# Kernel optimization log

Measured on AMD Instinct MI355X. Metric: run time of the kernel, lower is better.

The kernel has to match this reference:

```python
import jax, jax.numpy as jnp
import numpy as np

CARD = [3049, 10, 7, 3]
EMB = 16
HID = 64
COV = 10
B = 4096
S = 512
IN_DIM = 1 + COV + len(CARD) * EMB + 1  # 76


def setup_inputs() -> dict:
    key = jax.random.key(0)
    ks = jax.random.split(key, 12)
    target = jax.random.uniform(ks[0], (B, S), dtype=jnp.float32) * 100.0
    covariates = jax.random.normal(ks[1], (B, S, COV), dtype=jnp.float32)
    static_cats = jax.random.randint(ks[2], (B, len(CARD)), 0, 3)
    scale = jax.random.uniform(ks[3], (B, 1), dtype=jnp.float32) * 10.0 + 0.1
    emb0 = jax.random.normal(ks[4], (CARD[0], EMB), dtype=jnp.float32) * 0.1
    emb1 = jax.random.normal(ks[5], (CARD[1], EMB), dtype=jnp.float32) * 0.1
    emb2 = jax.random.normal(ks[6], (CARD[2], EMB), dtype=jnp.float32) * 0.1
    emb3 = jax.random.normal(ks[7], (CARD[3], EMB), dtype=jnp.float32) * 0.1
    w_ih = jax.random.normal(ks[8], (IN_DIM, 4 * HID), dtype=jnp.float32) / np.sqrt(IN_DIM)
    w_hh = jax.random.normal(ks[9], (HID, 4 * HID), dtype=jnp.float32) / np.sqrt(HID)
    bias = jnp.zeros((4 * HID,), dtype=jnp.float32)
    w_out = jax.random.normal(ks[10], (HID, 2), dtype=jnp.float32) / np.sqrt(HID)
    b_out = jnp.zeros((2,), dtype=jnp.float32)
    return dict(target=target, covariates=covariates, static_cats=static_cats,
                scale=scale, emb0=emb0, emb1=emb1, emb2=emb2, emb3=emb3,
                w_ih=w_ih, w_hh=w_hh, bias=bias, w_out=w_out, b_out=b_out)


def reference(target, covariates, static_cats, scale,
              emb0, emb1, emb2, emb3, w_ih, w_hh, bias, w_out, b_out):
    # static embedding concat: [B, 4*EMB]
    static_emb = jnp.concatenate([emb0[static_cats[:, 0]], emb1[static_cats[:, 1]],
                                  emb2[static_cats[:, 2]], emb3[static_cats[:, 3]]], axis=-1)
    log_scale = jnp.log1p(scale)                              # [B, 1]
    static_x = jnp.concatenate([static_emb, log_scale], -1)  # [B, 4*EMB+1]
    # teacher-forced previous scaled target: shifted target/scale, zero at t=0
    ps = target / jnp.maximum(scale, 1e-4)                    # [B, S]
    prev = jnp.concatenate([jnp.zeros_like(ps[:, :1]), ps[:, :-1]], axis=1)

    h0 = jnp.zeros((target.shape[0], w_hh.shape[0]), dtype=target.dtype)

    def step(carry, xs):
        h, c = carry
        p_t, cov_t = xs  # [B], [B, COV]
        x = jnp.concatenate([p_t[:, None], cov_t, static_x], axis=-1)  # [B, IN_DIM]
        gates = x @ w_ih + h @ w_hh + bias
        i, f, g, o = jnp.split(gates, 4, axis=-1)
        i = jax.nn.sigmoid(i)
        f = jax.nn.sigmoid(f)
        g = jnp.tanh(g)
        o = jax.nn.sigmoid(o)
        c = f * c + i * g
        h = o * jnp.tanh(c)
        raw = h @ w_out + b_out                    # [B, 2]
        mu_s = jax.nn.softplus(raw[:, 0]) + 1e-4   # [B]
        al = jax.nn.softplus(raw[:, 1]) + 1e-4     # [B]
        return (h, c), (mu_s, al)

    xs = (prev.T, jnp.swapaxes(covariates, 0, 1))  # time-major
    _, (mu_s, al) = jax.lax.scan(step, (h0, h0), xs)
    mus = mu_s.T * scale   # [B, S]
    alphas = al.T          # [B, S]
    return mus, alphas
```

## Files before the change

### kernel.cpp

```cpp
#include <hip/hip_runtime.h>

#define BB 4096
#define SS 512
#define NG 256
#define BT 16
#define NT 512
#define CH 32
#define HSTR 68
#define PSTR 16
#define SBSTR 264
#define OSTR 33

typedef __bf16 bf16_t;
typedef bf16_t bf16x8 __attribute__((ext_vector_type(8)));
typedef float  f32x4  __attribute__((ext_vector_type(4)));

__device__ __forceinline__ unsigned short f2bf(float x) {
    union { float f; unsigned u; } q{x};
    unsigned r = (q.u + 0x7fffu + ((q.u >> 16) & 1u)) >> 16;
    return (unsigned short)r;
}
__device__ __forceinline__ float bf2f(unsigned short s) {
    union { unsigned u; float f; } q{((unsigned)s) << 16};
    return q.f;
}
#define LOG2E 1.4426950408889634f
__device__ __forceinline__ float frcp_(float x)  { return __builtin_amdgcn_rcpf(x); }
__device__ __forceinline__ float fexp2_(float x) { return __builtin_amdgcn_exp2f(x); }
__device__ __forceinline__ float flog2_(float x) { return __builtin_amdgcn_logf(x); }
__device__ __forceinline__ float softplus_(float x){ return x > 20.0f ? x : 0.6931471805599453f * flog2_(1.0f + fexp2_(LOG2E * x)); }

__global__ __launch_bounds__(NT)
void deepar_kernel(const float* __restrict__ target, const float* __restrict__ cov,
                   const int* __restrict__ cats, const float* __restrict__ scale,
                   const float* __restrict__ emb0, const float* __restrict__ emb1,
                   const float* __restrict__ emb2, const float* __restrict__ emb3,
                   const float* __restrict__ w_ih, const float* __restrict__ w_hh,
                   const float* __restrict__ bias, const float* __restrict__ w_out,
                   const float* __restrict__ b_out, float* __restrict__ out)
{
    __shared__ __attribute__((aligned(16))) unsigned char smemA[2 * CH * BT * PSTR * 2];
    __shared__ __attribute__((aligned(16))) unsigned short hbuf[2][BT][HSTR];
    __shared__ float obuf[2][CH][OSTR];
    __shared__ float inv_s[BT], scl_s[BT];

    unsigned short* pcx   = (unsigned short*)smemA;
    float*          sbias = (float*)smemA;
    float*          sx    = (float*)(smemA + BT * SBSTR * 4);

    const int tid  = threadIdx.x;
    const int b0   = blockIdx.x * BT;
    const int lane = tid & 63;
    const int wv   = tid >> 6;
    const int qd   = lane >> 4;
    const int ln   = lane & 15;
    const bool is_compute = (wv < 4);
    const int tid2 = tid & 255;

    for (int i = tid; i < 2 * BT * HSTR; i += NT) ((unsigned short*)hbuf)[i] = 0;
    if (tid < BT) {
        float s = scale[b0 + tid];
        scl_s[tid] = s;
        inv_s[tid] = 1.0f / fmaxf(s, 1e-4f);
        sx[tid * 68 + 64] = log1pf(s);
    }
    if (tid < BT * 4) {
        int r = tid >> 2, e = tid & 3;
        int c = cats[(b0 + r) * 4 + e];
        const float* eb = (e == 0 ? emb0 : e == 1 ? emb1 : e == 2 ? emb2 : emb3);
        for (int j = 0; j < 16; ++j) sx[r * 68 + e * 16 + j] = eb[c * 16 + j];
    }
    __syncthreads();

    {
        const int n = tid & 255, half = tid >> 8;
        float bj = bias[n];
        float acc[8];
        #pragma unroll
        for (int r = 0; r < 8; ++r) acc[r] = bj;
        for (int k = 0; k < 65; ++k) {
            float w = w_ih[(11 + k) * NG + n];
            #pragma unroll
            for (int r = 0; r < 8; ++r) acc[r] += sx[(half * 8 + r) * 68 + k] * w;
        }
        #pragma unroll
        for (int r = 0; r < 8; ++r) sbias[(half * 8 + r) * SBSTR + n] = acc[r];
    }
    __syncthreads();

    bf16x8 bfrag[4][3];
    f32x4  sbf[4];
    if (is_compute) {
        #pragma unroll
        for (int ti = 0; ti < 4; ++ti) {
            const float gsc = (ti == 2) ? (-2.0f * LOG2E) : (-LOG2E);
            const int n = ln + 16 * (wv + 4 * ti);
            #pragma unroll
            for (int c = 0; c < 3; ++c) {
                #pragma unroll
                for (int j = 0; j < 8; ++j) {
                    int k = qd * 8 + 32 * c + j;
                    float w;
                    if (k < 64)                  w = w_hh[k * NG + n];
                    else if (k == 64 || k == 75) w = w_ih[n];
                    else if (k <= 74)            w = w_ih[(k - 64) * NG + n];
                    else                         w = 0.0f;
                    bfrag[ti][c][j] = (bf16_t)(w * gsc);
                }
            }
            #pragma unroll
            for (int r = 0; r < 4; ++r)
                sbf[ti][r] = sbias[(qd * 4 + r) * SBSTR + n] * gsc;
        }
    }

    bf16x8 wob0, wob1;
    f32x4  bC;
    float  scl4[4];
    #pragma unroll
    for (int j = 0; j < 8; ++j) {
        wob0[j] = (bf16_t)((ln < 2) ? w_out[(qd * 8 + j) * 2 + ln] : 0.0f);
        wob1[j] = (bf16_t)((ln < 2) ? w_out[(32 + qd * 8 + j) * 2 + ln] : 0.0f);
    }
    #pragma unroll
    for (int r = 0; r < 4; ++r) {
        bC[r]   = (ln < 2) ? b_out[ln] : 0.0f;
        scl4[r] = (ln == 0) ? scl_s[qd * 4 + r] : 1.0f;
    }

    __syncthreads();

    for (int i = tid; i < (2 * CH * BT * PSTR) / 2; i += NT) ((int*)smemA)[i] = 0;
    __syncthreads();

    if (tid < 256) {
        const int row = tid >> 4, i5 = tid & 15;
        const float* cr = cov + (size_t)(b0 + row) * (SS * 10);
        #pragma unroll
        for (int j = 0; j < 20; ++j) {
            int e = i5 + 16 * j, tp = e / 10, k = e - 10 * tp;
            pcx[((0 * CH + tp) * BT + row) * PSTR + 1 + k] = f2bf(cr[e]);
        }
        float pv0 = (i5 == 0) ? 0.0f : target[(size_t)(b0 + row) * SS + i5 - 1] * inv_s[row];
        float pv1 = target[(size_t)(b0 + row) * SS + i5 + 15] * inv_s[row];
        unsigned short m0 = f2bf(pv0), m1 = f2bf(pv1);
        pcx[((0 * CH + i5) * BT + row) * PSTR + 0]       = m0;
        pcx[((0 * CH + i5) * BT + row) * PSTR + 11]      = f2bf(pv0 - bf2f(m0));
        pcx[((0 * CH + i5 + 16) * BT + row) * PSTR + 0]  = m1;
        pcx[((0 * CH + i5 + 16) * BT + row) * PSTR + 11] = f2bf(pv1 - bf2f(m1));
    }
    __syncthreads();

    bf16x8 a2 = {};
    f32x4 acc_pre[4];
    if (is_compute) {
        if (qd < 2)
            a2 = *(const bf16x8*)&pcx[((0 * CH + 0) * BT + ln) * PSTR + qd * 8];
        #pragma unroll
        for (int ti = 0; ti < 4; ++ti)
            acc_pre[ti] = __builtin_amdgcn_mfma_f32_16x16x32_bf16(a2, bfrag[ti][2], sbf[ti], 0, 0, 0);
    }

    float cst[4] = {0.0f, 0.0f, 0.0f, 0.0f};
    float crg[20];
    #pragma unroll
    for (int j = 0; j < 20; ++j) crg[j] = 0.0f;
    float trg0 = 0.0f, trg1 = 0.0f;

    for (int t = 0; t < SS; ++t) {
        const int cur = t & 1, nxt = cur ^ 1;
        __syncthreads();

        if (is_compute) {
            const unsigned short* hb = &hbuf[cur][ln][0];
            bf16x8 a0 = *(const bf16x8*)(hb + qd * 8);
            bf16x8 a1 = *(const bf16x8*)(hb + 32 + qd * 8);

            f32x4 acc0 = __builtin_amdgcn_mfma_f32_16x16x32_bf16(a0, bfrag[0][0], acc_pre[0], 0, 0, 0);
            f32x4 acc1 = __builtin_amdgcn_mfma_f32_16x16x32_bf16(a0, bfrag[1][0], acc_pre[1], 0, 0, 0);
            f32x4 acc2 = __builtin_amdgcn_mfma_f32_16x16x32_bf16(a0, bfrag[2][0], acc_pre[2], 0, 0, 0);
            f32x4 acc3 = __builtin_amdgcn_mfma_f32_16x16x32_bf16(a0, bfrag[3][0], acc_pre[3], 0, 0, 0);
            acc0 = __builtin_amdgcn_mfma_f32_16x16x32_bf16(a1, bfrag[0][1], acc0, 0, 0, 0);
            acc1 = __builtin_amdgcn_mfma_f32_16x16x32_bf16(a1, bfrag[1][1], acc1, 0, 0, 0);
            acc2 = __builtin_amdgcn_mfma_f32_16x16x32_bf16(a1, bfrag[2][1], acc2, 0, 0, 0);
            acc3 = __builtin_amdgcn_mfma_f32_16x16x32_bf16(a1, bfrag[3][1], acc3, 0, 0, 0);

            if (t + 1 < SS && qd < 2)
                a2 = *(const bf16x8*)&pcx[((((t + 1) >> 5) & 1) * CH + ((t + 1) & 31)) * BT * PSTR
                                          + ln * PSTR + qd * 8];

            const int u = 16 * wv + ln;
            #pragma unroll
            for (int r = 0; r < 4; ++r) {
                float si = frcp_(1.0f + fexp2_(acc0[r]));
                float sf = frcp_(1.0f + fexp2_(acc1[r]));
                float tg = 2.0f * frcp_(1.0f + fexp2_(acc2[r])) - 1.0f;
                float so = frcp_(1.0f + fexp2_(acc3[r]));
                float cc = sf * cst[r] + si * tg;
                cst[r] = cc;
                float th = 2.0f * frcp_(1.0f + fexp2_((-2.0f * LOG2E) * cc)) - 1.0f;
                *(bf16_t*)&hbuf[nxt][qd * 4 + r][u] = (bf16_t)(so * th);
            }

            if (t + 1 < SS) {
                #pragma unroll
                for (int ti = 0; ti < 4; ++ti)
                    acc_pre[ti] = __builtin_amdgcn_mfma_f32_16x16x32_bf16(a2, bfrag[ti][2], sbf[ti], 0, 0, 0);
            }
        } else {
            if ((t & 31) == 0 && t < 480) {
                const int row = tid2 >> 4, i5 = tid2 & 15, t0n = t + CH;
                const float* cr = cov + (size_t)(b0 + row) * (SS * 10) + t0n * 10;
                #pragma unroll
                for (int j = 0; j < 20; ++j) crg[j] = cr[i5 + 16 * j];
                const float* tr = target + (size_t)(b0 + row) * SS + t0n + i5;
                trg0 = tr[-1];
                trg1 = tr[15];
            }

            if (wv == 4 && t > 0) {
                const unsigned short* hb = &hbuf[cur][ln][0];
                bf16x8 a0 = *(const bf16x8*)(hb + qd * 8);
                bf16x8 a1 = *(const bf16x8*)(hb + 32 + qd * 8);
                f32x4 hacc = __builtin_amdgcn_mfma_f32_16x16x32_bf16(a0, wob0, bC, 0, 0, 0);
                hacc = __builtin_amdgcn_mfma_f32_16x16x32_bf16(a1, wob1, hacc, 0, 0, 0);
                if (ln < 2) {
                    #pragma unroll
                    for (int r = 0; r < 4; ++r) {
                        float sp = softplus_(hacc[r]) + 1e-4f;
                        obuf[((t - 1) >> 5) & 1][(t - 1) & 31][ln * 16 + qd * 4 + r] = sp * scl4[r];
                    }
                }
            }

            if ((t & 31) == 16) {
                const int c = t >> 5;
                if (c < 15) {
                    const int row = tid2 >> 4, i5 = tid2 & 15, nb = (c + 1) & 1;
                    float pv0 = trg0 * inv_s[row];
                    float pv1 = trg1 * inv_s[row];
                    unsigned short m0 = f2bf(pv0), m1 = f2bf(pv1);
                    pcx[((nb * CH + i5) * BT + row) * PSTR + 0]       = m0;
                    pcx[((nb * CH + i5) * BT + row) * PSTR + 11]      = f2bf(pv0 - bf2f(m0));
                    pcx[((nb * CH + i5 + 16) * BT + row) * PSTR + 0]  = m1;
                    pcx[((nb * CH + i5 + 16) * BT + row) * PSTR + 11] = f2bf(pv1 - bf2f(m1));
                    #pragma unroll
                    for (int j = 0; j < 20; ++j) {
                        int e = i5 + 16 * j, tp = e / 10, k = e - 10 * tp;
                        pcx[((nb * CH + tp) * BT + row) * PSTR + 1 + k] = f2bf(crg[j]);
                    }
                }
                if (c >= 1) {
                    const int pb = (c - 1) & 1, t0p = (c - 1) << 5;
                    #pragma unroll
                    for (int h = 0; h < 4; ++h) {
                        int e = tid2 + 256 * h;
                        int tte = e & 31, rowe = (e >> 5) & 15, pe = e >> 9;
                        out[(pe ? (BB * SS) : 0) + (size_t)(b0 + rowe) * SS + t0p + tte] =
                            obuf[pb][tte][pe * 16 + rowe];
                    }
                }
            }
        }
    }

    __syncthreads();
    if (wv == 4) {
        const unsigned short* hb = &hbuf[0][ln][0];
        bf16x8 a0 = *(const bf16x8*)(hb + qd * 8);
        bf16x8 a1 = *(const bf16x8*)(hb + 32 + qd * 8);
        f32x4 hacc = __builtin_amdgcn_mfma_f32_16x16x32_bf16(a0, wob0, bC, 0, 0, 0);
        hacc = __builtin_amdgcn_mfma_f32_16x16x32_bf16(a1, wob1, hacc, 0, 0, 0);
        if (ln < 2) {
            #pragma unroll
            for (int r = 0; r < 4; ++r) {
                float sp = softplus_(hacc[r]) + 1e-4f;
                obuf[1][31][ln * 16 + qd * 4 + r] = sp * scl4[r];
            }
        }
    }
    __syncthreads();
    #pragma unroll
    for (int h = 0; h < 2; ++h) {
        int e = tid + NT * h;
        int tte = e & 31, rowe = (e >> 5) & 15, pe = e >> 9;
        out[(pe ? (BB * SS) : 0) + (size_t)(b0 + rowe) * SS + 480 + tte] =
            obuf[1][tte][pe * 16 + rowe];
    }
}

extern "C" void kernel_launch(void* const* d_in, const int* in_sizes, int n_in,
                              void* d_out, int out_size, void* d_ws, size_t ws_size,
                              hipStream_t stream) {
    deepar_kernel<<<BB / BT, NT, 0, stream>>>(
        (const float*)d_in[0], (const float*)d_in[1], (const int*)d_in[2],
        (const float*)d_in[3], (const float*)d_in[4], (const float*)d_in[5],
        (const float*)d_in[6], (const float*)d_in[7], (const float*)d_in[8],
        (const float*)d_in[9], (const float*)d_in[10], (const float*)d_in[11],
        (const float*)d_in[12], (float*)d_out);
}
```

Measured before the change: 496.8 us.

## Split LSTM gate nonlinearities across all eight waves and rotate output head

Every one of the eight waves now runs the recurrent MFMAs for its gate slice, so the matrix work is duplicated across wave pairs. The per-step transcendental cell update is split so each wave in a pair handles two of the four accumulator rows, halving the serial elementwise latency on the critical path. The output-head MFMA and softplus rotate across waves by timestep instead of sitting on a dedicated wave. The cost is redundant MFMA work, more register pressure on the former loader waves, and loader waves that must also join the compute step.

Result: slower. 592.7 us (+19.3%).

```diff
diff --git a/kernel.cpp b/kernel.cpp
--- a/kernel.cpp
+++ b/kernel.cpp
@@ -54,7 +54,7 @@
     const int wv   = tid >> 6;
     const int qd   = lane >> 4;
     const int ln   = lane & 15;
-    const bool is_compute = (wv < 4);
+    const int wvg  = wv & 3;
     const int tid2 = tid & 255;
 
     for (int i = tid; i < 2 * BT * HSTR; i += NT) ((unsigned short*)hbuf)[i] = 0;
@@ -90,11 +90,11 @@
 
     bf16x8 bfrag[4][3];
     f32x4  sbf[4];
-    if (is_compute) {
+    {
         #pragma unroll
         for (int ti = 0; ti < 4; ++ti) {
             const float gsc = (ti == 2) ? (-2.0f * LOG2E) : (-LOG2E);
-            const int n = ln + 16 * (wv + 4 * ti);
+            const int n = ln + 16 * (wvg + 4 * ti);
             #pragma unroll
             for (int c = 0; c < 3; ++c) {
                 #pragma unroll
@@ -153,7 +153,7 @@
 
     bf16x8 a2 = {};
     f32x4 acc_pre[4];
-    if (is_compute) {
+    {
         if (qd < 2)
             a2 = *(const bf16x8*)&pcx[((0 * CH + 0) * BT + ln) * PSTR + qd * 8];
         #pragma unroll
@@ -161,53 +161,68 @@
             acc_pre[ti] = __builtin_amdgcn_mfma_f32_16x16x32_bf16(a2, bfrag[ti][2], sbf[ti], 0, 0, 0);
     }
 
-    float cst[4] = {0.0f, 0.0f, 0.0f, 0.0f};
+    float cst[2] = {0.0f, 0.0f};
     float crg[20];
     #pragma unroll
     for (int j = 0; j < 20; ++j) crg[j] = 0.0f;
     float trg0 = 0.0f, trg1 = 0.0f;
 
+#define CELL(CI, RI)                                                            \
+    {                                                                           \
+        float si = frcp_(1.0f + fexp2_(acc0[RI]));                              \
+        float sf = frcp_(1.0f + fexp2_(acc1[RI]));                              \
+        float tg = 2.0f * frcp_(1.0f + fexp2_(acc2[RI])) - 1.0f;                \
+        float so = frcp_(1.0f + fexp2_(acc3[RI]));                              \
+        float cc = sf * cst[CI] + si * tg;                                      \
+        cst[CI] = cc;                                                           \
+        float th = 2.0f * frcp_(1.0f + fexp2_((-2.0f * LOG2E) * cc)) - 1.0f;    \
+        *(bf16_t*)&hbuf[nxt][qd * 4 + RI][u] = (bf16_t)(so * th);               \
+    }
+
     for (int t = 0; t < SS; ++t) {
         const int cur = t & 1, nxt = cur ^ 1;
         __syncthreads();
 
-        if (is_compute) {
-            const unsigned short* hb = &hbuf[cur][ln][0];
-            bf16x8 a0 = *(const bf16x8*)(hb + qd * 8);
-            bf16x8 a1 = *(const bf16x8*)(hb + 32 + qd * 8);
-
-            f32x4 acc0 = __builtin_amdgcn_mfma_f32_16x16x32_bf16(a0, bfrag[0][0], acc_pre[0], 0, 0, 0);
-            f32x4 acc1 = __builtin_amdgcn_mfma_f32_16x16x32_bf16(a0, bfrag[1][0], acc_pre[1], 0, 0, 0);
-            f32x4 acc2 = __builtin_amdgcn_mfma_f32_16x16x32_bf16(a0, bfrag[2][0], acc_pre[2], 0, 0, 0);
-            f32x4 acc3 = __builtin_amdgcn_mfma_f32_16x16x32_bf16(a0, bfrag[3][0], acc_pre[3], 0, 0, 0);
-            acc0 = __builtin_amdgcn_mfma_f32_16x16x32_bf16(a1, bfrag[0][1], acc0, 0, 0, 0);
-            acc1 = __builtin_amdgcn_mfma_f32_16x16x32_bf16(a1, bfrag[1][1], acc1, 0, 0, 0);
-            acc2 = __builtin_amdgcn_mfma_f32_16x16x32_bf16(a1, bfrag[2][1], acc2, 0, 0, 0);
-            acc3 = __builtin_amdgcn_mfma_f32_16x16x32_bf16(a1, bfrag[3][1], acc3, 0, 0, 0);
-
-            if (t + 1 < SS && qd < 2)
-                a2 = *(const bf16x8*)&pcx[((((t + 1) >> 5) & 1) * CH + ((t + 1) & 31)) * BT * PSTR
-                                          + ln * PSTR + qd * 8];
-
-            const int u = 16 * wv + ln;
-            #pragma unroll
-            for (int r = 0; r < 4; ++r) {
-                float si = frcp_(1.0f + fexp2_(acc0[r]));
-                float sf = frcp_(1.0f + fexp2_(acc1[r]));
-                float tg = 2.0f * frcp_(1.0f + fexp2_(acc2[r])) - 1.0f;
-                float so = frcp_(1.0f + fexp2_(acc3[r]));
-                float cc = sf * cst[r] + si * tg;
-                cst[r] = cc;
-                float th = 2.0f * frcp_(1.0f + fexp2_((-2.0f * LOG2E) * cc)) - 1.0f;
-                *(bf16_t*)&hbuf[nxt][qd * 4 + r][u] = (bf16_t)(so * th);
-            }
-
-            if (t + 1 < SS) {
+        const unsigned short* hb = &hbuf[cur][ln][0];
+        bf16x8 a0 = *(const bf16x8*)(hb + qd * 8);
+        bf16x8 a1 = *(const bf16x8*)(hb + 32 + qd * 8);
+
+        f32x4 acc0 = __builtin_amdgcn_mfma_f32_16x16x32_bf16(a0, bfrag[0][0], acc_pre[0], 0, 0, 0);
+        f32x4 acc1 = __builtin_amdgcn_mfma_f32_16x16x32_bf16(a0, bfrag[1][0], acc_pre[1], 0, 0, 0);
+        f32x4 acc2 = __builtin_amdgcn_mfma_f32_16x16x32_bf16(a0, bfrag[2][0], acc_pre[2], 0, 0, 0);
+        f32x4 acc3 = __builtin_amdgcn_mfma_f32_16x16x32_bf16(a0, bfrag[3][0], acc_pre[3], 0, 0, 0);
+        acc0 = __builtin_amdgcn_mfma_f32_16x16x32_bf16(a1, bfrag[0][1], acc0, 0, 0, 0);
+        acc1 = __builtin_amdgcn_mfma_f32_16x16x32_bf16(a1, bfrag[1][1], acc1, 0, 0, 0);
+        acc2 = __builtin_amdgcn_mfma_f32_16x16x32_bf16(a1, bfrag[2][1], acc2, 0, 0, 0);
+        acc3 = __builtin_amdgcn_mfma_f32_16x16x32_bf16(a1, bfrag[3][1], acc3, 0, 0, 0);
+
+        if (t + 1 < SS && qd < 2)
+            a2 = *(const bf16x8*)&pcx[((((t + 1) >> 5) & 1) * CH + ((t + 1) & 31)) * BT * PSTR
+                                      + ln * PSTR + qd * 8];
+
+        const int u = 16 * wvg + ln;
+        if (wv < 4) { CELL(0, 0); CELL(1, 1); }
+        else        { CELL(0, 2); CELL(1, 3); }
+
+        if (t > 0 && wv == (t & 7)) {
+            f32x4 hacc = __builtin_amdgcn_mfma_f32_16x16x32_bf16(a0, wob0, bC, 0, 0, 0);
+            hacc = __builtin_amdgcn_mfma_f32_16x16x32_bf16(a1, wob1, hacc, 0, 0, 0);
+            if (ln < 2) {
                 #pragma unroll
-                for (int ti = 0; ti < 4; ++ti)
-                    acc_pre[ti] = __builtin_amdgcn_mfma_f32_16x16x32_bf16(a2, bfrag[ti][2], sbf[ti], 0, 0, 0);
-            }
-        } else {
+                for (int r = 0; r < 4; ++r) {
+                    float sp = softplus_(hacc[r]) + 1e-4f;
+                    obuf[((t - 1) >> 5) & 1][(t - 1) & 31][ln * 16 + qd * 4 + r] = sp * scl4[r];
+                }
+            }
+        }
+
+        if (t + 1 < SS) {
+            #pragma unroll
+            for (int ti = 0; ti < 4; ++ti)
+                acc_pre[ti] = __builtin_amdgcn_mfma_f32_16x16x32_bf16(a2, bfrag[ti][2], sbf[ti], 0, 0, 0);
+        }
+
+        if (wv >= 4) {
             if ((t & 31) == 0 && t < 480) {
                 const int row = tid2 >> 4, i5 = tid2 & 15, t0n = t + CH;
                 const float* cr = cov + (size_t)(b0 + row) * (SS * 10) + t0n * 10;
@@ -216,21 +231,6 @@
                 const float* tr = target + (size_t)(b0 + row) * SS + t0n + i5;
                 trg0 = tr[-1];
                 trg1 = tr[15];
-            }
-
-            if (wv == 4 && t > 0) {
-                const unsigned short* hb = &hbuf[cur][ln][0];
-                bf16x8 a0 = *(const bf16x8*)(hb + qd * 8);
-                bf16x8 a1 = *(const bf16x8*)(hb + 32 + qd * 8);
-                f32x4 hacc = __builtin_amdgcn_mfma_f32_16x16x32_bf16(a0, wob0, bC, 0, 0, 0);
-                hacc = __builtin_amdgcn_mfma_f32_16x16x32_bf16(a1, wob1, hacc, 0, 0, 0);
-                if (ln < 2) {
-                    #pragma unroll
-                    for (int r = 0; r < 4; ++r) {
-                        float sp = softplus_(hacc[r]) + 1e-4f;
-                        obuf[((t - 1) >> 5) & 1][(t - 1) & 31][ln * 16 + qd * 4 + r] = sp * scl4[r];
-                    }
-                }
             }
 
             if ((t & 31) == 16) {
```

## Drop producer warps, fold I/O and output head into compute waves

Applied to the files above, without the earlier changes.

Shrinks the block from 8 waves to 4 by removing the dedicated loader/output-head waves. The compute waves now do the covariate prefetch, staging and output stores themselves. The output head is rotated across waves by t&3, and the input MFMA is moved inside the step instead of being software-pipelined ahead. The gate math is also rewritten algebraically to share one reciprocal across the sigmoid/tanh combinations, which cuts transcendental ops per step but puts global loads and the extra MFMA on the serial critical path.

New measurement: 560.9 us. 12.9% more time.

```diff
diff --git a/kernel.cpp b/kernel.cpp
--- a/kernel.cpp
+++ b/kernel.cpp
@@ -4,7 +4,7 @@
 #define SS 512
 #define NG 256
 #define BT 16
-#define NT 512
+#define NT 256
 #define CH 32
 #define HSTR 68
 #define PSTR 16
@@ -30,7 +30,7 @@
 __device__ __forceinline__ float flog2_(float x) { return __builtin_amdgcn_logf(x); }
 __device__ __forceinline__ float softplus_(float x){ return x > 20.0f ? x : 0.6931471805599453f * flog2_(1.0f + fexp2_(LOG2E * x)); }
 
-__global__ __launch_bounds__(NT)
+__global__ __launch_bounds__(NT, 1)
 void deepar_kernel(const float* __restrict__ target, const float* __restrict__ cov,
                    const int* __restrict__ cats, const float* __restrict__ scale,
                    const float* __restrict__ emb0, const float* __restrict__ emb1,
@@ -54,8 +54,6 @@
     const int wv   = tid >> 6;
     const int qd   = lane >> 4;
     const int ln   = lane & 15;
-    const bool is_compute = (wv < 4);
-    const int tid2 = tid & 255;
 
     for (int i = tid; i < 2 * BT * HSTR; i += NT) ((unsigned short*)hbuf)[i] = 0;
     if (tid < BT) {
@@ -73,24 +71,24 @@
     __syncthreads();
 
     {
-        const int n = tid & 255, half = tid >> 8;
+        const int n = tid;
         float bj = bias[n];
-        float acc[8];
-        #pragma unroll
-        for (int r = 0; r < 8; ++r) acc[r] = bj;
+        float acc[BT];
+        #pragma unroll
+        for (int r = 0; r < BT; ++r) acc[r] = bj;
         for (int k = 0; k < 65; ++k) {
             float w = w_ih[(11 + k) * NG + n];
             #pragma unroll
-            for (int r = 0; r < 8; ++r) acc[r] += sx[(half * 8 + r) * 68 + k] * w;
-        }
-        #pragma unroll
-        for (int r = 0; r < 8; ++r) sbias[(half * 8 + r) * SBSTR + n] = acc[r];
+            for (int r = 0; r < BT; ++r) acc[r] += sx[r * 68 + k] * w;
+        }
+        #pragma unroll
+        for (int r = 0; r < BT; ++r) sbias[r * SBSTR + n] = acc[r];
     }
     __syncthreads();
 
     bf16x8 bfrag[4][3];
     f32x4  sbf[4];
-    if (is_compute) {
+    {
         #pragma unroll
         for (int ti = 0; ti < 4; ++ti) {
             const float gsc = (ti == 2) ? (-2.0f * LOG2E) : (-LOG2E);
@@ -133,7 +131,7 @@
     for (int i = tid; i < (2 * CH * BT * PSTR) / 2; i += NT) ((int*)smemA)[i] = 0;
     __syncthreads();
 
-    if (tid < 256) {
+    {
         const int row = tid >> 4, i5 = tid & 15;
         const float* cr = cov + (size_t)(b0 + row) * (SS * 10);
         #pragma unroll
@@ -152,14 +150,8 @@
     __syncthreads();
 
     bf16x8 a2 = {};
-    f32x4 acc_pre[4];
-    if (is_compute) {
-        if (qd < 2)
-            a2 = *(const bf16x8*)&pcx[((0 * CH + 0) * BT + ln) * PSTR + qd * 8];
-        #pragma unroll
-        for (int ti = 0; ti < 4; ++ti)
-            acc_pre[ti] = __builtin_amdgcn_mfma_f32_16x16x32_bf16(a2, bfrag[ti][2], sbf[ti], 0, 0, 0);
-    }
+    if (qd < 2)
+        a2 = *(const bf16x8*)&pcx[((0 * CH + 0) * BT + ln) * PSTR + qd * 8];
 
     float cst[4] = {0.0f, 0.0f, 0.0f, 0.0f};
     float crg[20];
@@ -171,101 +163,98 @@
         const int cur = t & 1, nxt = cur ^ 1;
         __syncthreads();
 
-        if (is_compute) {
-            const unsigned short* hb = &hbuf[cur][ln][0];
-            bf16x8 a0 = *(const bf16x8*)(hb + qd * 8);
-            bf16x8 a1 = *(const bf16x8*)(hb + 32 + qd * 8);
-
-            f32x4 acc0 = __builtin_amdgcn_mfma_f32_16x16x32_bf16(a0, bfrag[0][0], acc_pre[0], 0, 0, 0);
-            f32x4 acc1 = __builtin_amdgcn_mfma_f32_16x16x32_bf16(a0, bfrag[1][0], acc_pre[1], 0, 0, 0);
-            f32x4 acc2 = __builtin_amdgcn_mfma_f32_16x16x32_bf16(a0, bfrag[2][0], acc_pre[2], 0, 0, 0);
-            f32x4 acc3 = __builtin_amdgcn_mfma_f32_16x16x32_bf16(a0, bfrag[3][0], acc_pre[3], 0, 0, 0);
-            acc0 = __builtin_amdgcn_mfma_f32_16x16x32_bf16(a1, bfrag[0][1], acc0, 0, 0, 0);
-            acc1 = __builtin_amdgcn_mfma_f32_16x16x32_bf16(a1, bfrag[1][1], acc1, 0, 0, 0);
-            acc2 = __builtin_amdgcn_mfma_f32_16x16x32_bf16(a1, bfrag[2][1], acc2, 0, 0, 0);
-            acc3 = __builtin_amdgcn_mfma_f32_16x16x32_bf16(a1, bfrag[3][1], acc3, 0, 0, 0);
-
-            if (t + 1 < SS && qd < 2)
-                a2 = *(const bf16x8*)&pcx[((((t + 1) >> 5) & 1) * CH + ((t + 1) & 31)) * BT * PSTR
-                                          + ln * PSTR + qd * 8];
-
-            const int u = 16 * wv + ln;
-            #pragma unroll
-            for (int r = 0; r < 4; ++r) {
-                float si = frcp_(1.0f + fexp2_(acc0[r]));
-                float sf = frcp_(1.0f + fexp2_(acc1[r]));
-                float tg = 2.0f * frcp_(1.0f + fexp2_(acc2[r])) - 1.0f;
-                float so = frcp_(1.0f + fexp2_(acc3[r]));
-                float cc = sf * cst[r] + si * tg;
-                cst[r] = cc;
-                float th = 2.0f * frcp_(1.0f + fexp2_((-2.0f * LOG2E) * cc)) - 1.0f;
-                *(bf16_t*)&hbuf[nxt][qd * 4 + r][u] = (bf16_t)(so * th);
-            }
-
-            if (t + 1 < SS) {
-                #pragma unroll
-                for (int ti = 0; ti < 4; ++ti)
-                    acc_pre[ti] = __builtin_amdgcn_mfma_f32_16x16x32_bf16(a2, bfrag[ti][2], sbf[ti], 0, 0, 0);
-            }
-        } else {
-            if ((t & 31) == 0 && t < 480) {
-                const int row = tid2 >> 4, i5 = tid2 & 15, t0n = t + CH;
-                const float* cr = cov + (size_t)(b0 + row) * (SS * 10) + t0n * 10;
-                #pragma unroll
-                for (int j = 0; j < 20; ++j) crg[j] = cr[i5 + 16 * j];
-                const float* tr = target + (size_t)(b0 + row) * SS + t0n + i5;
-                trg0 = tr[-1];
-                trg1 = tr[15];
-            }
-
-            if (wv == 4 && t > 0) {
-                const unsigned short* hb = &hbuf[cur][ln][0];
-                bf16x8 a0 = *(const bf16x8*)(hb + qd * 8);
-                bf16x8 a1 = *(const bf16x8*)(hb + 32 + qd * 8);
-                f32x4 hacc = __builtin_amdgcn_mfma_f32_16x16x32_bf16(a0, wob0, bC, 0, 0, 0);
-                hacc = __builtin_amdgcn_mfma_f32_16x16x32_bf16(a1, wob1, hacc, 0, 0, 0);
-                if (ln < 2) {
-                    #pragma unroll
-                    for (int r = 0; r < 4; ++r) {
-                        float sp = softplus_(hacc[r]) + 1e-4f;
-                        obuf[((t - 1) >> 5) & 1][(t - 1) & 31][ln * 16 + qd * 4 + r] = sp * scl4[r];
-                    }
-                }
-            }
-
-            if ((t & 31) == 16) {
-                const int c = t >> 5;
-                if (c < 15) {
-                    const int row = tid2 >> 4, i5 = tid2 & 15, nb = (c + 1) & 1;
-                    float pv0 = trg0 * inv_s[row];
-                    float pv1 = trg1 * inv_s[row];
-                    unsigned short m0 = f2bf(pv0), m1 = f2bf(pv1);
-                    pcx[((nb * CH + i5) * BT + row) * PSTR + 0]       = m0;
-                    pcx[((nb * CH + i5) * BT + row) * PSTR + 11]      = f2bf(pv0 - bf2f(m0));
-                    pcx[((nb * CH + i5 + 16) * BT + row) * PSTR + 0]  = m1;
-                    pcx[((nb * CH + i5 + 16) * BT + row) * PSTR + 11] = f2bf(pv1 - bf2f(m1));
-                    #pragma unroll
-                    for (int j = 0; j < 20; ++j) {
-                        int e = i5 + 16 * j, tp = e / 10, k = e - 10 * tp;
-                        pcx[((nb * CH + tp) * BT + row) * PSTR + 1 + k] = f2bf(crg[j]);
-                    }
-                }
-                if (c >= 1) {
-                    const int pb = (c - 1) & 1, t0p = (c - 1) << 5;
-                    #pragma unroll
-                    for (int h = 0; h < 4; ++h) {
-                        int e = tid2 + 256 * h;
-                        int tte = e & 31, rowe = (e >> 5) & 15, pe = e >> 9;
-                        out[(pe ? (BB * SS) : 0) + (size_t)(b0 + rowe) * SS + t0p + tte] =
-                            obuf[pb][tte][pe * 16 + rowe];
-                    }
-                }
-            }
-        }
-    }
-
-    __syncthreads();
-    if (wv == 4) {
+        const unsigned short* hb = &hbuf[cur][ln][0];
+        bf16x8 a0 = *(const bf16x8*)(hb + qd * 8);
+        bf16x8 a1 = *(const bf16x8*)(hb + 32 + qd * 8);
+
+        f32x4 acc0 = __builtin_amdgcn_mfma_f32_16x16x32_bf16(a2, bfrag[0][2], sbf[0], 0, 0, 0);
+        f32x4 acc1 = __builtin_amdgcn_mfma_f32_16x16x32_bf16(a2, bfrag[1][2], sbf[1], 0, 0, 0);
+        f32x4 acc2 = __builtin_amdgcn_mfma_f32_16x16x32_bf16(a2, bfrag[2][2], sbf[2], 0, 0, 0);
+        f32x4 acc3 = __builtin_amdgcn_mfma_f32_16x16x32_bf16(a2, bfrag[3][2], sbf[3], 0, 0, 0);
+
+        acc0 = __builtin_amdgcn_mfma_f32_16x16x32_bf16(a0, bfrag[0][0], acc0, 0, 0, 0);
+        acc1 = __builtin_amdgcn_mfma_f32_16x16x32_bf16(a0, bfrag[1][0], acc1, 0, 0, 0);
+        acc2 = __builtin_amdgcn_mfma_f32_16x16x32_bf16(a0, bfrag[2][0], acc2, 0, 0, 0);
+        acc3 = __builtin_amdgcn_mfma_f32_16x16x32_bf16(a0, bfrag[3][0], acc3, 0, 0, 0);
+        acc0 = __builtin_amdgcn_mfma_f32_16x16x32_bf16(a1, bfrag[0][1], acc0, 0, 0, 0);
+        acc1 = __builtin_amdgcn_mfma_f32_16x16x32_bf16(a1, bfrag[1][1], acc1, 0, 0, 0);
+        acc2 = __builtin_amdgcn_mfma_f32_16x16x32_bf16(a1, bfrag[2][1], acc2, 0, 0, 0);
+        acc3 = __builtin_amdgcn_mfma_f32_16x16x32_bf16(a1, bfrag[3][1], acc3, 0, 0, 0);
+
+        if (t + 1 < SS && qd < 2)
+            a2 = *(const bf16x8*)&pcx[((((t + 1) >> 5) & 1) * CH + ((t + 1) & 31)) * BT * PSTR
+                                      + ln * PSTR + qd * 8];
+
+        const int u = 16 * wv + ln;
+        #pragma unroll
+        for (int r = 0; r < 4; ++r) {
+            float a  = fexp2_(fminf(acc0[r], 30.0f));
+            float fe = fexp2_(fminf(acc1[r], 30.0f));
+            float bb = fexp2_(fminf(acc2[r], 30.0f));
+            float oe = fexp2_(fminf(acc3[r], 30.0f));
+            float p  = (1.0f + a) * (1.0f + bb);
+            float q  = 1.0f + fe;
+            float cc = (cst[r] * p + (1.0f - bb) * q) * frcp_(p * q);
+            cst[r] = cc;
+            float d  = fexp2_(fminf((-2.0f * LOG2E) * cc, 30.0f));
+            float hv = (1.0f - d) * frcp_((1.0f + oe) * (1.0f + d));
+            *(bf16_t*)&hbuf[nxt][qd * 4 + r][u] = (bf16_t)hv;
+        }
+
+        if (t > 0 && wv == (t & 3)) {
+            f32x4 hacc = __builtin_amdgcn_mfma_f32_16x16x32_bf16(a0, wob0, bC, 0, 0, 0);
+            hacc = __builtin_amdgcn_mfma_f32_16x16x32_bf16(a1, wob1, hacc, 0, 0, 0);
+            if (ln < 2) {
+                #pragma unroll
+                for (int r = 0; r < 4; ++r) {
+                    float sp = softplus_(hacc[r]) + 1e-4f;
+                    obuf[((t - 1) >> 5) & 1][(t - 1) & 31][ln * 16 + qd * 4 + r] = sp * scl4[r];
+                }
+            }
+        }
+
+        if ((t & 31) == 0 && t < 480) {
+            const int row = tid >> 4, i5 = tid & 15, t0n = t + CH;
+            const float* cr = cov + (size_t)(b0 + row) * (SS * 10) + t0n * 10;
+            #pragma unroll
+            for (int j = 0; j < 20; ++j) crg[j] = cr[i5 + 16 * j];
+            const float* tr = target + (size_t)(b0 + row) * SS + t0n + i5;
+            trg0 = tr[-1];
+            trg1 = tr[15];
+        }
+
+        if ((t & 31) == 16) {
+            const int c = t >> 5;
+            if (c < 15) {
+                const int row = tid >> 4, i5 = tid & 15, nb = (c + 1) & 1;
+                float pv0 = trg0 * inv_s[row];
+                float pv1 = trg1 * inv_s[row];
+                unsigned short m0 = f2bf(pv0), m1 = f2bf(pv1);
+                pcx[((nb * CH + i5) * BT + row) * PSTR + 0]       = m0;
+                pcx[((nb * CH + i5) * BT + row) * PSTR + 11]      = f2bf(pv0 - bf2f(m0));
+                pcx[((nb * CH + i5 + 16) * BT + row) * PSTR + 0]  = m1;
+                pcx[((nb * CH + i5 + 16) * BT + row) * PSTR + 11] = f2bf(pv1 - bf2f(m1));
+                #pragma unroll
+                for (int j = 0; j < 20; ++j) {
+                    int e = i5 + 16 * j, tp = e / 10, k = e - 10 * tp;
+                    pcx[((nb * CH + tp) * BT + row) * PSTR + 1 + k] = f2bf(crg[j]);
+                }
+            }
+            if (c >= 1) {
+                const int pb = (c - 1) & 1, t0p = (c - 1) << 5;
+                #pragma unroll
+                for (int h = 0; h < 4; ++h) {
+                    int e = tid + NT * h;
+                    int tte = e & 31, rowe = (e >> 5) & 15, pe = e >> 9;
+                    out[(pe ? (BB * SS) : 0) + (size_t)(b0 + rowe) * SS + t0p + tte] =
+                        obuf[pb][tte][pe * 16 + rowe];
+                }
+            }
+        }
+    }
+
+    __syncthreads();
+    if (wv == 0) {
         const unsigned short* hb = &hbuf[0][ln][0];
         bf16x8 a0 = *(const bf16x8*)(hb + qd * 8);
         bf16x8 a1 = *(const bf16x8*)(hb + 32 + qd * 8);
@@ -281,7 +270,7 @@
     }
     __syncthreads();
     #pragma unroll
-    for (int h = 0; h < 2; ++h) {
+    for (int h = 0; h < 4; ++h) {
         int e = tid + NT * h;
         int tte = e & 31, rowe = (e >> 5) & 15, pe = e >> 9;
         out[(pe ? (BB * SS) : 0) + (size_t)(b0 + rowe) * SS + 480 + tte] =
```
